# Kernel optimization log

Measured on AMD Instinct MI355X. Metric: run time of the kernel, lower is better.

Reference implementation:

```python
import jax, jax.numpy as jnp
import numpy as np

B, V, T, C, HIN, WIN = 1, 6, 3, 256, 32, 32
NH = 8
LN_EPS = 1e-5


def setup_inputs() -> dict:
    key = jax.random.key(0)
    ks = jax.random.split(key, 14)
    s = 0.02
    lim = 1.0 / np.sqrt(C)
    def lin_w(k):
        return jax.random.uniform(k, (C, C), jnp.float32, -lim, lim)
    return {
        "history_feats": jax.random.normal(ks[0], (B, V, T, C, HIN, WIN), jnp.float32),
        "query_embed": jax.random.normal(ks[1], (1, C, 1, 1), jnp.float32) * s,
        "camera_pos_embed": jax.random.normal(ks[2], (V, C), jnp.float32) * s,
        "temporal_pos_embed": jax.random.normal(ks[3], (T, C), jnp.float32) * s,
        "spatial_pos_embed": jax.random.normal(ks[4], (1, C, 1, 1), jnp.float32) * s,
        "q_w": lin_w(ks[5]), "q_b": jnp.zeros((C,), jnp.float32),
        "k_w": lin_w(ks[6]), "k_b": jnp.zeros((C,), jnp.float32),
        "v_w": lin_w(ks[7]), "v_b": jnp.zeros((C,), jnp.float32),
        "o_w": lin_w(ks[8]), "o_b": jnp.zeros((C,), jnp.float32),
        "ln_g": jnp.ones((C,), jnp.float32),
        "ln_b": jnp.zeros((C,), jnp.float32),
        "query_cam_idx": 0,
        "H": 32,
        "W": 32,
    }


def reference(history_feats, query_embed, camera_pos_embed, temporal_pos_embed,
              spatial_pos_embed, q_w, q_b, k_w, k_b, v_w, v_b, o_w, o_b,
              ln_g, ln_b, query_cam_idx, H, W):
    B_, V_, T_, C_, Hin, Win = history_feats.shape
    dh = C_ // NH
    # --- build query: [B, H*W, C] ---
    q = query_embed + camera_pos_embed[query_cam_idx][None, :, None, None] + spatial_pos_embed
    q = jnp.broadcast_to(q, (B_, C_, H, W)).reshape(B_, C_, H * W).transpose(0, 2, 1)
    kv = (history_feats
          + temporal_pos_embed[None, None, :, :, None, None]
          + camera_pos_embed[None, :, None, :, None, None])
    kv = kv.transpose(0, 1, 2, 4, 5, 3).reshape(B_, V_ * T_ * Hin * Win, C_)
    # --- projections (torch Linear: x @ W.T + b) ---
    qp = q @ q_w.T + q_b
    kp = kv @ k_w.T + k_b
    vp = kv @ v_w.T + v_b
    # --- split heads: [B, NH, L, dh] ---
    qh = qp.reshape(B_, H * W, NH, dh).transpose(0, 2, 1, 3)
    kh = kp.reshape(B_, -1, NH, dh).transpose(0, 2, 1, 3)
    vh = vp.reshape(B_, -1, NH, dh).transpose(0, 2, 1, 3)
    scale = float(dh) ** -0.5
    attn = jax.nn.softmax(jnp.einsum('bhqd,bhkd->bhqk', qh, kh) * scale, axis=-1)
    out = jnp.einsum('bhqk,bhkd->bhqd', attn, vh)
    out = out.transpose(0, 2, 1, 3).reshape(B_, H * W, C_)
    out = out @ o_w.T + o_b
    # --- LayerNorm over channel dim ---
    mu = out.mean(-1, keepdims=True)
    var = ((out - mu) ** 2).mean(-1, keepdims=True)
    out = (out - mu) * jax.lax.rsqrt(var + LN_EPS) * ln_g + ln_b
    return out.transpose(0, 2, 1).reshape(B_, C_, H, W)
```

## Files before the change

kernel.cpp:

```cpp
#include <hip/hip_runtime.h>

typedef const float* fcp;

#define C_    256
#define NH_   8
#define DH_   32
#define VT_   18
#define HWK   1024
#define L_    (VT_*HWK)
#define SCALE_ 0.17677669529663687f

#define QP_OFF   256
#define EMB_OFF  512
#define PM_OFF   5120
#define PS_OFF   7424
#define CTX_OFF  9728
#define Y_OFF    11776
#define Z_OFF    12032
#define SC_OFF   12288
#define PEX_OFF  159744

__device__ __forceinline__ float blockReduceSum256(float v){
  __shared__ float red[4];
  #pragma unroll
  for (int off = 32; off; off >>= 1) v += __shfl_xor(v, off, 64);
  const int lane = threadIdx.x & 63, w = threadIdx.x >> 6;
  __syncthreads();
  if (lane == 0) red[w] = v;
  __syncthreads();
  return red[0] + red[1] + red[2] + red[3];
}

__global__ void k_qp(fcp qe, fcp cam, fcp tpe, fcp spe, const int* __restrict__ cidx,
                     fcp qw, fcp qb, float* __restrict__ ws){
  __shared__ float qvS[C_];
  const int r = blockIdx.x, t = threadIdx.x;
  const int ci = cidx[0];
  qvS[t] = qe[t] + cam[ci*C_ + t] + spe[t];
  __syncthreads();
  if (r < VT_){
    const int v = r/3, tt = r - v*3;
    ws[EMB_OFF + r*C_ + t] = tpe[tt*C_ + t] + cam[v*C_ + t];
  }
  if (r == 255){
    #pragma unroll
    for (int i = 0; i < 8; i++) ws[CTX_OFF + i*C_ + t] = 0.f;
  }
  float v = qw[r*C_ + t] * qvS[t];
  v = blockReduceSum256(v);
  if (t == 0) ws[QP_OFF + r] = v + qb[r];
}

__global__ void k_scores(fcp feats, fcp kw, fcp kb, float* __restrict__ ws){
  __shared__ __align__(16) float wf[C_*8];
  __shared__ float qpS[C_];
  __shared__ float bbS[8];
  __shared__ float redS[32];
  __shared__ float basef[8];
  __shared__ float pred[4*512];
  const int bid = blockIdx.x, vt = bid >> 4, sc = bid & 15, t = threadIdx.x;

  qpS[t] = ws[QP_OFF + t];
  __syncthreads();
  {
    const int c = t;
    float facc[8] = {0,0,0,0,0,0,0,0};
    #pragma unroll
    for (int h = 0; h < 8; h++){
      #pragma unroll 8
      for (int d = 0; d < DH_; d++)
        facc[h] += qpS[h*DH_ + d] * kw[(size_t)(h*DH_ + d)*C_ + c];
    }
    #pragma unroll
    for (int h = 0; h < 8; h++) wf[c*8 + h] = SCALE_ * facc[h];
    if (t < 8){
      float bb = 0.f;
      for (int d = 0; d < DH_; d++) bb += qpS[t*DH_ + d] * kb[t*DH_ + d];
      bbS[t] = SCALE_ * bb;
    }
  }
  __syncthreads();
  {
    const float e = ws[EMB_OFF + vt*C_ + t];
    const float4 wa = *(const float4*)&wf[t*8];
    const float4 wb = *(const float4*)&wf[t*8 + 4];
    float pb[8] = {e*wa.x, e*wa.y, e*wa.z, e*wa.w, e*wb.x, e*wb.y, e*wb.z, e*wb.w};
    #pragma unroll
    for (int h = 0; h < 8; h++){
      float v = pb[h];
      #pragma unroll
      for (int off = 32; off; off >>= 1) v += __shfl_xor(v, off, 64);
      if ((t & 63) == 0) redS[(t >> 6)*8 + h] = v;
    }
    __syncthreads();
    if (t < 8) basef[t] = redS[t] + redS[8+t] + redS[16+t] + redS[24+t] + bbS[t];
  }
  __syncthreads();
  const int s = t & 63, cg = t >> 6;
  const int gb = vt*HWK + sc*64;
  fcp fp = feats + ((size_t)vt*C_ + cg*64)*HWK + sc*64 + s;
  float acc[8] = {0,0,0,0,0,0,0,0};
  #pragma unroll 8
  for (int i = 0; i < 64; i++){
    const float fv = fp[(size_t)i*HWK];
    const float4 wa = *(const float4*)&wf[(cg*64+i)*8];
    const float4 wb = *(const float4*)&wf[(cg*64+i)*8 + 4];
    acc[0] += fv*wa.x; acc[1] += fv*wa.y; acc[2] += fv*wa.z; acc[3] += fv*wa.w;
    acc[4] += fv*wb.x; acc[5] += fv*wb.y; acc[6] += fv*wb.z; acc[7] += fv*wb.w;
  }
  #pragma unroll
  for (int h = 0; h < 8; h++) pred[cg*512 + h*64 + s] = acc[h];
  __syncthreads();
  const int h1 = t >> 6;
  float s1 = pred[t]     + pred[512+t]     + pred[1024+t]     + pred[1536+t]     + basef[h1];
  float s2 = pred[256+t] + pred[512+256+t] + pred[1024+256+t] + pred[1536+256+t] + basef[h1+4];
  ws[SC_OFF + (size_t)h1*L_ + gb + s]     = s1;
  ws[SC_OFF + (size_t)(h1+4)*L_ + gb + s] = s2;
  float m1 = s1, m2 = s2;
  #pragma unroll
  for (int off = 32; off; off >>= 1){
    m1 = fmaxf(m1, __shfl_xor(m1, off, 64));
    m2 = fmaxf(m2, __shfl_xor(m2, off, 64));
  }
  if (s == 0){
    ws[PM_OFF + bid*8 + h1]     = m1;
    ws[PM_OFF + bid*8 + h1 + 4] = m2;
  }
}

__global__ void k_pexp(float* __restrict__ ws){
  __shared__ float pm2[256];
  __shared__ float mS[8];
  const int bid = blockIdx.x, vt = bid >> 4, sc = bid & 15, t = threadIdx.x;
  {
    float v = -1e30f;
    #pragma unroll
    for (int k = 0; k < 9; k++) v = fmaxf(v, ws[PM_OFF + t + 256*k]);
    pm2[t] = v;
    __syncthreads();
    if (t < 64){
      const int h2 = t & 7, q = t >> 3;
      float m = fmaxf(fmaxf(pm2[q*32 + h2], pm2[q*32 + 8 + h2]),
                      fmaxf(pm2[q*32 + 16 + h2], pm2[q*32 + 24 + h2]));
      m = fmaxf(m, __shfl_xor(m, 8, 64));
      m = fmaxf(m, __shfl_xor(m, 16, 64));
      m = fmaxf(m, __shfl_xor(m, 32, 64));
      if (t < 8) mS[t] = m;
    }
  }
  __syncthreads();
  const int s = t & 63, hh = t >> 6;
  const int g = vt*HWK + sc*64 + s;
  const int h0 = hh*2;
  float e0 = __expf(ws[SC_OFF + (size_t)h0*L_ + g]     - mS[h0]);
  float e1 = __expf(ws[SC_OFF + (size_t)(h0+1)*L_ + g] - mS[h0+1]);
  *(float2*)(ws + PEX_OFF + (size_t)g*8 + h0) = make_float2(e0, e1);
  float v0 = e0, v1 = e1;
  #pragma unroll
  for (int off = 32; off; off >>= 1){
    v0 += __shfl_xor(v0, off, 64);
    v1 += __shfl_xor(v1, off, 64);
  }
  if (s == 0){
    ws[PS_OFF + bid*8 + h0]     = v0;
    ws[PS_OFF + bid*8 + h0 + 1] = v1;
  }
}

__global__ void k_ctx(fcp feats, float* __restrict__ ws){
  const int bid = blockIdx.x;
  const int vt = bid / 64, r = bid - vt*64, cc = r & 15, ssi = r >> 4;
  const int t = threadIdx.x, wv = t >> 6, lane = t & 63;
  const int c0 = cc*16 + wv*4;
  fcp fb = feats + (size_t)vt*C_*HWK + ssi*256;
  const float* pexb = ws + PEX_OFF + ((size_t)vt*HWK + ssi*256)*8;
  float acc[4][8];
  #pragma unroll
  for (int j = 0; j < 4; j++)
    #pragma unroll
    for (int h = 0; h < 8; h++) acc[j][h] = 0.f;

  #pragma unroll
  for (int step = 0; step < 4; step++){
    const int s = step*64 + lane;
    const float4 pa = *(const float4*)(pexb + (size_t)s*8);
    const float4 pb = *(const float4*)(pexb + (size_t)s*8 + 4);
    #pragma unroll
    for (int j = 0; j < 4; j++){
      const float fv = fb[(size_t)(c0 + j)*HWK + s];
      acc[j][0] += fv*pa.x; acc[j][1] += fv*pa.y; acc[j][2] += fv*pa.z; acc[j][3] += fv*pa.w;
      acc[j][4] += fv*pb.x; acc[j][5] += fv*pb.y; acc[j][6] += fv*pb.z; acc[j][7] += fv*pb.w;
    }
  }
  #pragma unroll
  for (int j = 0; j < 4; j++)
    #pragma unroll
    for (int h = 0; h < 8; h++){
      float v = acc[j][h];
      #pragma unroll
      for (int off = 32; off; off >>= 1) v += __shfl_xor(v, off, 64);
      if (lane == j*8 + h) atomicAdd(ws + CTX_OFF + h*C_ + c0 + j, v);
    }
}

__global__ void k_vproj(fcp vw, fcp vb, float* __restrict__ ws){
  __shared__ float psS[288*8];
  const int r = blockIdx.x, t = threadIdx.x, h = r >> 5;
  for (int i = t; i < 288*8; i += 256) psS[i] = ws[PS_OFF + i];
  __syncthreads();
  float denom = 0.f, embP = 0.f;
  for (int vt = 0; vt < VT_; vt++){
    float P = 0.f;
    #pragma unroll
    for (int sc2 = 0; sc2 < 16; sc2++) P += psS[(vt*16 + sc2)*8 + h];
    denom += P;
    embP  += ws[EMB_OFF + vt*C_ + t] * P;
  }
  const float ctxn = (ws[CTX_OFF + h*C_ + t] + embP) / denom;
  float v = vw[(size_t)r*C_ + t] * ctxn;
  v = blockReduceSum256(v);
  if (t == 0) ws[Y_OFF + r] = v + vb[r];
}

__global__ void k_oproj(fcp ow, fcp ob, float* __restrict__ ws){
  const int r = blockIdx.x, t = threadIdx.x;
  float v = ow[(size_t)r*C_ + t] * ws[Y_OFF + t];
  v = blockReduceSum256(v);
  if (t == 0) ws[Z_OFF + r] = v + ob[r];
}

__global__ void k_out(fcp lng, fcp lnb, const float* __restrict__ ws,
                      float* __restrict__ out, int hw){
  const int c = blockIdx.x, t = threadIdx.x;
  const float z = ws[Z_OFF + t];
  const float s  = blockReduceSum256(z);
  const float s2 = blockReduceSum256(z*z);
  const float mu = s * (1.f/C_);
  const float var = s2 * (1.f/C_) - mu*mu;
  const float rs = rsqrtf(var + 1e-5f);
  const float fin = (ws[Z_OFF + c] - mu) * rs * lng[c] + lnb[c];
  float4 pk = make_float4(fin, fin, fin, fin);
  ((float4*)(out + (size_t)c*hw))[t] = pk;
}

extern "C" void kernel_launch(void* const* d_in, const int* in_sizes, int n_in,
                              void* d_out, int out_size, void* d_ws, size_t ws_size,
                              hipStream_t stream) {
  fcp feats = (fcp)d_in[0];
  fcp qe    = (fcp)d_in[1];
  fcp cam   = (fcp)d_in[2];
  fcp tpe   = (fcp)d_in[3];
  fcp spe   = (fcp)d_in[4];
  fcp qw    = (fcp)d_in[5];
  fcp qb    = (fcp)d_in[6];
  fcp kw    = (fcp)d_in[7];
  fcp kb    = (fcp)d_in[8];
  fcp vw    = (fcp)d_in[9];
  fcp vb    = (fcp)d_in[10];
  fcp ow    = (fcp)d_in[11];
  fcp ob    = (fcp)d_in[12];
  fcp lng   = (fcp)d_in[13];
  fcp lnb   = (fcp)d_in[14];
  const int* cidx = (const int*)d_in[15];
  float* ws = (float*)d_ws;
  float* out = (float*)d_out;
  const int hw = out_size / C_;

  k_qp    <<<256,  256, 0, stream>>>(qe, cam, tpe, spe, cidx, qw, qb, ws);
  k_scores<<<288,  256, 0, stream>>>(feats, kw, kb, ws);
  k_pexp  <<<288,  256, 0, stream>>>(ws);
  k_ctx   <<<1152, 256, 0, stream>>>(feats, ws);
  k_vproj <<<256,  256, 0, stream>>>(vw, vb, ws);
  k_oproj <<<256,  256, 0, stream>>>(ow, ob, ws);
  k_out   <<<256,  256, 0, stream>>>(lng, lnb, ws, out, hw);
}
```

Measured before the change: 167.3 us.

## Fold query-key weights once, drop softmax max pass, fuse tail projections

Computes the query projection and the folded query-key weight vector once in a small 18-block kernel, instead of redoing the fold in every score block. The score kernel now exponentiates directly without subtracting a global max, which removes the separate max/exp kernel and the round-trip of raw scores through memory. The v-projection, o-projection and LayerNorm are merged into one tail kernel that each block computes redundantly, cutting launches from seven to four. Skipping the max subtraction risks overflow if scores are large. Making every tail block recompute both full matvecs adds redundant weight reads.

New measurement: 216.7 us. 29.6% more time.

```diff
diff --git a/kernel.cpp b/kernel.cpp
--- a/kernel.cpp
+++ b/kernel.cpp
@@ -10,15 +10,12 @@
 #define L_    (VT_*HWK)
 #define SCALE_ 0.17677669529663687f
 
-#define QP_OFF   256
-#define EMB_OFF  512
-#define PM_OFF   5120
-#define PS_OFF   7424
-#define CTX_OFF  9728
-#define Y_OFF    11776
-#define Z_OFF    12032
-#define SC_OFF   12288
-#define PEX_OFF  159744
+#define EMB_OFF  0
+#define WF_OFF   4608
+#define BB_OFF   6656
+#define PS_OFF   6720
+#define CTX_OFF  9088
+#define PEX_OFF  11264
 
 __device__ __forceinline__ float blockReduceSum256(float v){
   __shared__ float red[4];
@@ -31,54 +28,56 @@
   return red[0] + red[1] + red[2] + red[3];
 }
 
-__global__ void k_qp(fcp qe, fcp cam, fcp tpe, fcp spe, const int* __restrict__ cidx,
-                     fcp qw, fcp qb, float* __restrict__ ws){
+__global__ void k_fold(fcp qe, fcp cam, fcp tpe, fcp spe, const int* __restrict__ cidx,
+                       fcp qw, fcp qb, fcp kw, fcp kb, float* __restrict__ ws){
   __shared__ float qvS[C_];
-  const int r = blockIdx.x, t = threadIdx.x;
+  __shared__ float qpS[DH_];
+  const int b = blockIdx.x, t = threadIdx.x, lane = t & 63, wv = t >> 6;
   const int ci = cidx[0];
   qvS[t] = qe[t] + cam[ci*C_ + t] + spe[t];
-  __syncthreads();
-  if (r < VT_){
-    const int v = r/3, tt = r - v*3;
-    ws[EMB_OFF + r*C_ + t] = tpe[tt*C_ + t] + cam[v*C_ + t];
-  }
-  if (r == 255){
+  {
+    const int v = b/3, tt = b - v*3;
+    ws[EMB_OFF + b*C_ + t] = tpe[tt*C_ + t] + cam[v*C_ + t];
+  }
+  if (b == 17){
     #pragma unroll
     for (int i = 0; i < 8; i++) ws[CTX_OFF + i*C_ + t] = 0.f;
   }
-  float v = qw[r*C_ + t] * qvS[t];
-  v = blockReduceSum256(v);
-  if (t == 0) ws[QP_OFF + r] = v + qb[r];
-}
-
-__global__ void k_scores(fcp feats, fcp kw, fcp kb, float* __restrict__ ws){
+  __syncthreads();
+  if (b < 8){
+    #pragma unroll
+    for (int i = 0; i < 8; i++){
+      const int r = b*DH_ + wv*8 + i;
+      fcp qr = qw + (size_t)r*C_;
+      float v = qr[lane]*qvS[lane] + qr[64+lane]*qvS[64+lane]
+              + qr[128+lane]*qvS[128+lane] + qr[192+lane]*qvS[192+lane];
+      #pragma unroll
+      for (int off = 32; off; off >>= 1) v += __shfl_xor(v, off, 64);
+      if (lane == 0) qpS[wv*8 + i] = v + qb[r];
+    }
+    __syncthreads();
+    float acc = 0.f;
+    #pragma unroll 8
+    for (int d = 0; d < DH_; d++)
+      acc += qpS[d] * kw[(size_t)(b*DH_ + d)*C_ + t];
+    ws[WF_OFF + b*C_ + t] = SCALE_ * acc;
+    if (t == 0){
+      float bb = 0.f;
+      for (int d = 0; d < DH_; d++) bb += qpS[d] * kb[b*DH_ + d];
+      ws[BB_OFF + b] = SCALE_ * bb;
+    }
+  }
+}
+
+__global__ void k_scores(fcp feats, float* __restrict__ ws){
   __shared__ __align__(16) float wf[C_*8];
-  __shared__ float qpS[C_];
-  __shared__ float bbS[8];
   __shared__ float redS[32];
   __shared__ float basef[8];
   __shared__ float pred[4*512];
   const int bid = blockIdx.x, vt = bid >> 4, sc = bid & 15, t = threadIdx.x;
 
-  qpS[t] = ws[QP_OFF + t];
-  __syncthreads();
-  {
-    const int c = t;
-    float facc[8] = {0,0,0,0,0,0,0,0};
-    #pragma unroll
-    for (int h = 0; h < 8; h++){
-      #pragma unroll 8
-      for (int d = 0; d < DH_; d++)
-        facc[h] += qpS[h*DH_ + d] * kw[(size_t)(h*DH_ + d)*C_ + c];
-    }
-    #pragma unroll
-    for (int h = 0; h < 8; h++) wf[c*8 + h] = SCALE_ * facc[h];
-    if (t < 8){
-      float bb = 0.f;
-      for (int d = 0; d < DH_; d++) bb += qpS[t*DH_ + d] * kb[t*DH_ + d];
-      bbS[t] = SCALE_ * bb;
-    }
-  }
+  #pragma unroll
+  for (int h = 0; h < 8; h++) wf[t*8 + h] = ws[WF_OFF + h*C_ + t];
   __syncthreads();
   {
     const float e = ws[EMB_OFF + vt*C_ + t];
@@ -93,7 +92,7 @@
       if ((t & 63) == 0) redS[(t >> 6)*8 + h] = v;
     }
     __syncthreads();
-    if (t < 8) basef[t] = redS[t] + redS[8+t] + redS[16+t] + redS[24+t] + bbS[t];
+    if (t < 8) basef[t] = redS[t] + redS[8+t] + redS[16+t] + redS[24+t] + ws[BB_OFF + t];
   }
   __syncthreads();
   const int s = t & 63, cg = t >> 6;
@@ -111,59 +110,22 @@
   #pragma unroll
   for (int h = 0; h < 8; h++) pred[cg*512 + h*64 + s] = acc[h];
   __syncthreads();
-  const int h1 = t >> 6;
+  const int h1 = t >> 6, tok = t & 63;
   float s1 = pred[t]     + pred[512+t]     + pred[1024+t]     + pred[1536+t]     + basef[h1];
   float s2 = pred[256+t] + pred[512+256+t] + pred[1024+256+t] + pred[1536+256+t] + basef[h1+4];
-  ws[SC_OFF + (size_t)h1*L_ + gb + s]     = s1;
-  ws[SC_OFF + (size_t)(h1+4)*L_ + gb + s] = s2;
-  float m1 = s1, m2 = s2;
+  const float e1 = __expf(s1), e2 = __expf(s2);
+  float* px = ws + PEX_OFF + (size_t)(gb + tok)*8;
+  px[h1]     = e1;
+  px[h1 + 4] = e2;
+  float v1 = e1, v2 = e2;
   #pragma unroll
   for (int off = 32; off; off >>= 1){
-    m1 = fmaxf(m1, __shfl_xor(m1, off, 64));
-    m2 = fmaxf(m2, __shfl_xor(m2, off, 64));
-  }
-  if (s == 0){
-    ws[PM_OFF + bid*8 + h1]     = m1;
-    ws[PM_OFF + bid*8 + h1 + 4] = m2;
-  }
-}
-
-__global__ void k_pexp(float* __restrict__ ws){
-  __shared__ float pm2[256];
-  __shared__ float mS[8];
-  const int bid = blockIdx.x, vt = bid >> 4, sc = bid & 15, t = threadIdx.x;
-  {
-    float v = -1e30f;
-    #pragma unroll
-    for (int k = 0; k < 9; k++) v = fmaxf(v, ws[PM_OFF + t + 256*k]);
-    pm2[t] = v;
-    __syncthreads();
-    if (t < 64){
-      const int h2 = t & 7, q = t >> 3;
-      float m = fmaxf(fmaxf(pm2[q*32 + h2], pm2[q*32 + 8 + h2]),
-                      fmaxf(pm2[q*32 + 16 + h2], pm2[q*32 + 24 + h2]));
-      m = fmaxf(m, __shfl_xor(m, 8, 64));
-      m = fmaxf(m, __shfl_xor(m, 16, 64));
-      m = fmaxf(m, __shfl_xor(m, 32, 64));
-      if (t < 8) mS[t] = m;
-    }
-  }
-  __syncthreads();
-  const int s = t & 63, hh = t >> 6;
-  const int g = vt*HWK + sc*64 + s;
-  const int h0 = hh*2;
-  float e0 = __expf(ws[SC_OFF + (size_t)h0*L_ + g]     - mS[h0]);
-  float e1 = __expf(ws[SC_OFF + (size_t)(h0+1)*L_ + g] - mS[h0+1]);
-  *(float2*)(ws + PEX_OFF + (size_t)g*8 + h0) = make_float2(e0, e1);
-  float v0 = e0, v1 = e1;
-  #pragma unroll
-  for (int off = 32; off; off >>= 1){
-    v0 += __shfl_xor(v0, off, 64);
     v1 += __shfl_xor(v1, off, 64);
-  }
-  if (s == 0){
-    ws[PS_OFF + bid*8 + h0]     = v0;
-    ws[PS_OFF + bid*8 + h0 + 1] = v1;
+    v2 += __shfl_xor(v2, off, 64);
+  }
+  if (tok == 0){
+    ws[PS_OFF + bid*8 + h1]     = v1;
+    ws[PS_OFF + bid*8 + h1 + 4] = v2;
   }
 }
 
@@ -203,42 +165,71 @@
     }
 }
 
-__global__ void k_vproj(fcp vw, fcp vb, float* __restrict__ ws){
-  __shared__ float psS[288*8];
-  const int r = blockIdx.x, t = threadIdx.x, h = r >> 5;
-  for (int i = t; i < 288*8; i += 256) psS[i] = ws[PS_OFF + i];
-  __syncthreads();
-  float denom = 0.f, embP = 0.f;
-  for (int vt = 0; vt < VT_; vt++){
-    float P = 0.f;
-    #pragma unroll
-    for (int sc2 = 0; sc2 < 16; sc2++) P += psS[(vt*16 + sc2)*8 + h];
-    denom += P;
-    embP  += ws[EMB_OFF + vt*C_ + t] * P;
-  }
-  const float ctxn = (ws[CTX_OFF + h*C_ + t] + embP) / denom;
-  float v = vw[(size_t)r*C_ + t] * ctxn;
-  v = blockReduceSum256(v);
-  if (t == 0) ws[Y_OFF + r] = v + vb[r];
-}
-
-__global__ void k_oproj(fcp ow, fcp ob, float* __restrict__ ws){
-  const int r = blockIdx.x, t = threadIdx.x;
-  float v = ow[(size_t)r*C_ + t] * ws[Y_OFF + t];
-  v = blockReduceSum256(v);
-  if (t == 0) ws[Z_OFF + r] = v + ob[r];
-}
-
-__global__ void k_out(fcp lng, fcp lnb, const float* __restrict__ ws,
-                      float* __restrict__ out, int hw){
-  const int c = blockIdx.x, t = threadIdx.x;
-  const float z = ws[Z_OFF + t];
+__global__ void k_tail(fcp vw, fcp vb, fcp ow, fcp ob, fcp lng, fcp lnb,
+                       const float* __restrict__ ws, float* __restrict__ out, int hw){
+  __shared__ float Pvt[VT_*8];
+  __shared__ float denomS[8];
+  __shared__ __align__(16) float ctxnS[8*C_];
+  __shared__ float yS[C_];
+  __shared__ float zS[C_];
+  const int t = threadIdx.x, lane = t & 63, wv = t >> 6;
+  if (t < VT_*8){
+    const int vt = t >> 3, h = t & 7;
+    float p = 0.f;
+    #pragma unroll
+    for (int s2 = 0; s2 < 16; s2++) p += ws[PS_OFF + (vt*16 + s2)*8 + h];
+    Pvt[t] = p;
+  }
+  __syncthreads();
+  if (t < 8){
+    float d = 0.f;
+    #pragma unroll
+    for (int vt = 0; vt < VT_; vt++) d += Pvt[vt*8 + t];
+    denomS[t] = d;
+  }
+  __syncthreads();
+  {
+    float embP[8] = {0,0,0,0,0,0,0,0};
+    #pragma unroll 2
+    for (int vt = 0; vt < VT_; vt++){
+      const float e = ws[EMB_OFF + vt*C_ + t];
+      #pragma unroll
+      for (int h = 0; h < 8; h++) embP[h] += e * Pvt[vt*8 + h];
+    }
+    #pragma unroll
+    for (int h = 0; h < 8; h++)
+      ctxnS[h*C_ + t] = (ws[CTX_OFF + h*C_ + t] + embP[h]) / denomS[h];
+  }
+  __syncthreads();
+  for (int i = 0; i < 64; i++){
+    const int r = wv*64 + i;
+    const float* cn = ctxnS + (r >> 5)*C_;
+    fcp vr = vw + (size_t)r*C_;
+    float v = vr[lane]*cn[lane] + vr[64+lane]*cn[64+lane]
+            + vr[128+lane]*cn[128+lane] + vr[192+lane]*cn[192+lane];
+    #pragma unroll
+    for (int off = 32; off; off >>= 1) v += __shfl_xor(v, off, 64);
+    if (lane == 0) yS[r] = v + vb[r];
+  }
+  __syncthreads();
+  for (int i = 0; i < 64; i++){
+    const int o = wv*64 + i;
+    fcp orow = ow + (size_t)o*C_;
+    float v = orow[lane]*yS[lane] + orow[64+lane]*yS[64+lane]
+            + orow[128+lane]*yS[128+lane] + orow[192+lane]*yS[192+lane];
+    #pragma unroll
+    for (int off = 32; off; off >>= 1) v += __shfl_xor(v, off, 64);
+    if (lane == 0) zS[o] = v + ob[o];
+  }
+  __syncthreads();
+  const float z = zS[t];
   const float s  = blockReduceSum256(z);
   const float s2 = blockReduceSum256(z*z);
   const float mu = s * (1.f/C_);
   const float var = s2 * (1.f/C_) - mu*mu;
   const float rs = rsqrtf(var + 1e-5f);
-  const float fin = (ws[Z_OFF + c] - mu) * rs * lng[c] + lnb[c];
+  const int c = blockIdx.x;
+  const float fin = (zS[c] - mu) * rs * lng[c] + lnb[c];
   float4 pk = make_float4(fin, fin, fin, fin);
   ((float4*)(out + (size_t)c*hw))[t] = pk;
 }
@@ -266,11 +257,8 @@
   float* out = (float*)d_out;
   const int hw = out_size / C_;
 
-  k_qp    <<<256,  256, 0, stream>>>(qe, cam, tpe, spe, cidx, qw, qb, ws);
-  k_scores<<<288,  256, 0, stream>>>(feats, kw, kb, ws);
-  k_pexp  <<<288,  256, 0, stream>>>(ws);
+  k_fold  <<<18,   256, 0, stream>>>(qe, cam, tpe, spe, cidx, qw, qb, kw, kb, ws);
+  k_scores<<<288,  256, 0, stream>>>(feats, ws);
   k_ctx   <<<1152, 256, 0, stream>>>(feats, ws);
-  k_vproj <<<256,  256, 0, stream>>>(vw, vb, ws);
-  k_oproj <<<256,  256, 0, stream>>>(ow, ob, ws);
-  k_out   <<<256,  256, 0, stream>>>(lng, lnb, ws, out, hw);
-}
+  k_tail  <<<256,  256, 0, stream>>>(vw, vb, ow, ob, lng, lnb, ws, out, hw);
+}
```
